# Kernel tuning notes

Hardware: AMD Instinct MI355X
Metric: run time of the kernel (lower is better)

## Reference

```python
import jax, jax.numpy as jnp
import numpy as np
from jax import lax

H = 1024       # hidden_size
I = 1024       # intermediate_size (per expert)
E = 16         # num_experts
TOP_K = 4      # num_active_experts


def setup_inputs() -> dict:
    key = jax.random.key(0)
    ks = jax.random.split(key, 9)
    std_gate = 0.02 / (E ** 0.5)
    return {
        "hidden_states": jax.random.normal(ks[0], (1, 2048, H), jnp.float32),
        "gate_w": jax.random.normal(ks[1], (E, H), jnp.float32) * std_gate,
        "expert_bias": jnp.zeros((E,), jnp.float32),
        "w1": jax.random.normal(ks[2], (E, I, H), jnp.float32) * 0.02,
        "w2": jax.random.normal(ks[3], (E, H, I), jnp.float32) * 0.02,
        "w3": jax.random.normal(ks[4], (E, I, H), jnp.float32) * 0.02,
        "sw1": jax.random.normal(ks[5], (I, H), jnp.float32) * 0.02,
        "sw2": jax.random.normal(ks[6], (H, I), jnp.float32) * 0.02,
        "sw3": jax.random.normal(ks[7], (I, H), jnp.float32) * 0.02,
    }


def _swiglu(x, wg, wd, wu):
    # Swish(x W1^T) * (x W3^T) then W2^T
    return (jax.nn.silu(x @ wg.T) * (x @ wu.T)) @ wd.T


def reference(hidden_states, gate_w, expert_bias, w1, w2, w3, sw1, sw2, sw3):
    B, S, Hd = hidden_states.shape
    x = hidden_states.reshape(-1, Hd)              # [T, H]
    T = x.shape[0]

    # ---- Router ----
    router_logits = x @ gate_w.T                   # [T, E]
    biased = router_logits + expert_bias           # loss-free balancing bias
    _, sel = lax.top_k(biased, TOP_K)              # [T, K] indices from biased logits
    raw = jnp.take_along_axis(router_logits, sel, axis=-1)  # weights from UNbiased logits
    rw = jax.nn.softmax(raw.astype(jnp.float32), axis=-1).astype(x.dtype)  # [T, K]

    # Dense combine weights g[t, e] = routing weight if e selected else 0
    g = jnp.zeros((T, E), x.dtype).at[jnp.arange(T)[:, None], sel].add(rw)

    # ---- Routed experts (mathematically equal to grouped dispatch) ----
    routed = jnp.zeros_like(x)
    for e in range(E):  # fixed small expert loop
        routed = routed + g[:, e:e + 1] * _swiglu(x, w1[e], w2[e], w3[e])

    # ---- Shared expert ----
    shared = _swiglu(x, sw1, sw2, sw3)

    out = (shared + routed).reshape(B, S, Hd)      # dropout p=0 -> identity
    return out
```

## Files before the change

### kernel.cpp

```cpp
#include <hip/hip_runtime.h>
#include <cstddef>
#include <cstdint>

#define T_TOK 2048
#define HD 1024
#define ID 1024
#define NE 16
#define TOPK 4
#define BM 128
#define BN 128
#define BK 32
#define MT_MAX 96
#define SLOT_CAP (MT_MAX * BM)

typedef float f32x4 __attribute__((ext_vector_type(4)));
typedef __bf16 bf16x8 __attribute__((ext_vector_type(8)));
typedef __bf16 bf16x4 __attribute__((ext_vector_type(4)));

#define WS_TILE_E 256
#define WS_LOGITS 4096
#define WS_SLOT_TOK (WS_LOGITS + T_TOK * NE * 4)
#define WS_SLOT_W (WS_SLOT_TOK + SLOT_CAP * 4)
#define WS_H1 (WS_SLOT_W + SLOT_CAP * 4)
#define WS_XB (WS_H1 + (size_t)SLOT_CAP * ID * 2)
#define WS_W1B (WS_XB + (size_t)T_TOK * HD * 2)
#define EXSZ ((size_t)ID * HD)

__device__ __forceinline__ f32x4 mfma16(bf16x8 a, bf16x8 b, f32x4 c) {
  return __builtin_amdgcn_mfma_f32_16x16x32_bf16(a, b, c, 0, 0, 0);
}

__device__ __forceinline__ bf16x4 pack4(f32x4 a) {
  bf16x4 o;
  o[0] = (__bf16)a[0]; o[1] = (__bf16)a[1]; o[2] = (__bf16)a[2]; o[3] = (__bf16)a[3];
  return o;
}

__device__ __forceinline__ void gload16(const __bf16* g, __bf16* l) {
  __builtin_amdgcn_global_load_lds(
      (const __attribute__((address_space(1))) uint32_t*)g,
      (__attribute__((address_space(3))) uint32_t*)l, 16, 0, 0);
}

__device__ __forceinline__ void cvt_chunk(const float* __restrict__ src,
                                          __bf16* __restrict__ dst, size_t off,
                                          int tid) {
  const f32x4* p = (const f32x4*)src + off + tid;
  __bf16* q = dst + 4 * (off + tid);
  f32x4 v0 = __builtin_nontemporal_load(p);
  f32x4 v1 = __builtin_nontemporal_load(p + 256);
  f32x4 v2 = __builtin_nontemporal_load(p + 512);
  f32x4 v3 = __builtin_nontemporal_load(p + 768);
  f32x4 v4 = __builtin_nontemporal_load(p + 1024);
  f32x4 v5 = __builtin_nontemporal_load(p + 1280);
  f32x4 v6 = __builtin_nontemporal_load(p + 1536);
  f32x4 v7 = __builtin_nontemporal_load(p + 1792);
  *(bf16x4*)(q + 0 * 1024) = pack4(v0);
  *(bf16x4*)(q + 1 * 1024) = pack4(v1);
  *(bf16x4*)(q + 2 * 1024) = pack4(v2);
  *(bf16x4*)(q + 3 * 1024) = pack4(v3);
  *(bf16x4*)(q + 4 * 1024) = pack4(v4);
  *(bf16x4*)(q + 5 * 1024) = pack4(v5);
  *(bf16x4*)(q + 6 * 1024) = pack4(v6);
  *(bf16x4*)(q + 7 * 1024) = pack4(v7);
}

#define W4 ((size_t)1 << 22)
#define S4 ((size_t)1 << 18)
#define X4 ((size_t)1 << 19)
#define CVT4_TOTAL (2 * W4 + 2 * S4 + X4)
#define NCHUNK (CVT4_TOTAL / 2048)
#define CVT_GRID 2048
#define LOGITS_BLOCKS (T_TOK / 4)

__global__ __launch_bounds__(256) void fused_pre(
    const float* __restrict__ w1, const float* __restrict__ w3,
    const float* __restrict__ sw1, const float* __restrict__ sw3,
    const float* __restrict__ x, __bf16* __restrict__ w1b,
    __bf16* __restrict__ w3b, __bf16* __restrict__ xb,
    const float* __restrict__ gw, float* __restrict__ logits) {
  int tid = threadIdx.x;
  if ((int)blockIdx.x < LOGITS_BLOCKS) {
    int wv = tid >> 6;
    int lane = tid & 63;
    int tok = blockIdx.x * 4 + wv;
    int e = lane >> 2;
    int q = lane & 3;
    const float4* xr = (const float4*)(x + (size_t)tok * HD) + q * 64;
    const float4* wr = (const float4*)(gw + (size_t)e * HD) + q * 64;
    float s0 = 0.f, s1 = 0.f;
#pragma unroll 8
    for (int i = 0; i < 64; i += 2) {
      float4 a0 = xr[i], w0 = wr[i];
      float4 a1 = xr[i + 1], w1v = wr[i + 1];
      s0 += a0.x * w0.x + a0.y * w0.y + a0.z * w0.z + a0.w * w0.w;
      s1 += a1.x * w1v.x + a1.y * w1v.y + a1.z * w1v.z + a1.w * w1v.w;
    }
    float s = s0 + s1;
    s += __shfl_xor(s, 1);
    s += __shfl_xor(s, 2);
    if (q == 0) logits[(size_t)tok * NE + e] = s;
    return;
  }
  size_t b = blockIdx.x - LOGITS_BLOCKS;
  for (size_t c = b; c < NCHUNK; c += CVT_GRID) {
    size_t f = c * 2048;
    const float* src;
    __bf16* dst;
    size_t off;
    if (f < W4) { src = w1; dst = w1b; off = f; }
    else if (f < 2 * W4) { src = w3; dst = w3b; off = f - W4; }
    else if (f < 2 * W4 + S4) { src = sw1; dst = w1b + 16 * EXSZ; off = f - 2 * W4; }
    else if (f < 2 * W4 + 2 * S4) { src = sw3; dst = w3b + 16 * EXSZ; off = f - 2 * W4 - S4; }
    else { src = x; dst = xb; off = f - 2 * W4 - 2 * S4; }
    cvt_chunk(src, dst, off, tid);
  }
}

__global__ __launch_bounds__(256) void router_finish(
    const float* __restrict__ logits, const float* __restrict__ bias,
    int* __restrict__ tile_e, int* __restrict__ slot_tok,
    float* __restrict__ slot_w) {
  __shared__ int hist[NE];
  __shared__ int soff[NE + 1];
  __shared__ int fillp[NE];
  __shared__ unsigned lsel[T_TOK];
  __shared__ float4 lw4[T_TOK];

  int tid = threadIdx.x;
  if (tid < NE) { hist[tid] = 0; fillp[tid] = 0; }
  __syncthreads();

  float bb[NE];
#pragma unroll
  for (int e = 0; e < NE; ++e) bb[e] = bias[e];

  for (int j = 0; j < T_TOK / 256; ++j) {
    int t = tid + 256 * j;
    float lg[NE];
    const float4* lp = (const float4*)(logits + (size_t)t * NE);
#pragma unroll
    for (int q = 0; q < 4; ++q) {
      float4 v = lp[q];
      lg[4 * q] = v.x; lg[4 * q + 1] = v.y; lg[4 * q + 2] = v.z; lg[4 * q + 3] = v.w;
    }
    float b[NE];
#pragma unroll
    for (int e = 0; e < NE; ++e) b[e] = lg[e] + bb[e];

    int selk[TOPK];
    float raw[TOPK];
    unsigned used = 0;
#pragma unroll
    for (int k = 0; k < TOPK; ++k) {
      float best = -3.4e38f;
      int bi = 0;
#pragma unroll
      for (int e = 0; e < NE; ++e) {
        if (!((used >> e) & 1) && b[e] > best) { best = b[e]; bi = e; }
      }
      used |= (1u << bi);
      selk[k] = bi;
      raw[k] = lg[bi];
    }
    float m = raw[0];
#pragma unroll
    for (int k = 1; k < TOPK; ++k) m = fmaxf(m, raw[k]);
    float s = 0.f;
    float w[TOPK];
#pragma unroll
    for (int k = 0; k < TOPK; ++k) { w[k] = __expf(raw[k] - m); s += w[k]; }
    float inv = 1.f / s;
    lsel[t] = (unsigned)selk[0] | ((unsigned)selk[1] << 8) |
              ((unsigned)selk[2] << 16) | ((unsigned)selk[3] << 24);
    lw4[t] = make_float4(w[0] * inv, w[1] * inv, w[2] * inv, w[3] * inv);
#pragma unroll
    for (int k = 0; k < TOPK; ++k) atomicAdd(&hist[selk[k]], 1);
  }
  __syncthreads();

  if (tid == 0) {
    int o = 0;
    for (int e = 0; e < NE; ++e) { soff[e] = o; o += (hist[e] + BM - 1) & ~(BM - 1); }
    soff[NE] = o;
  }
  __syncthreads();
  int shared_base = soff[NE];
  int total = shared_base + T_TOK;
  for (int tt = tid; tt < MT_MAX; tt += 256) {
    int base = tt * BM;
    int ee = -1;
    if (base < shared_base) {
      ee = 0;
#pragma unroll
      for (int q = 1; q < NE; ++q) if (base >= soff[q]) ee = q;
    } else if (base < total) {
      ee = NE;
    }
    tile_e[tt] = ee;
  }

  for (int j = 0; j < T_TOK / 256; ++j) {
    int t = tid + 256 * j;
    unsigned ps = lsel[t];
    float4 wv = lw4[t];
    int e0 = ps & 255, e1 = (ps >> 8) & 255, e2 = (ps >> 16) & 255, e3 = ps >> 24;
    int p0 = atomicAdd(&fillp[e0], 1);
    slot_tok[soff[e0] + p0] = t; slot_w[soff[e0] + p0] = wv.x;
    int p1 = atomicAdd(&fillp[e1], 1);
    slot_tok[soff[e1] + p1] = t; slot_w[soff[e1] + p1] = wv.y;
    int p2 = atomicAdd(&fillp[e2], 1);
    slot_tok[soff[e2] + p2] = t; slot_w[soff[e2] + p2] = wv.z;
    int p3 = atomicAdd(&fillp[e3], 1);
    slot_tok[soff[e3] + p3] = t; slot_w[soff[e3] + p3] = wv.w;
  }

  for (int s = tid; s < shared_base; s += 256) {
    int e = 0;
#pragma unroll
    for (int q = 1; q < NE; ++q) if (s >= soff[q]) e = q;
    if (s >= soff[e] + hist[e]) { slot_tok[s] = -1; slot_w[s] = 0.f; }
  }
  for (int s = shared_base + tid; s < total; s += 256) {
    slot_tok[s] = s - shared_base;
    slot_w[s] = 1.0f;
  }
}

#define P1_BLOCKS (8 * MT_MAX)
#define W2CHUNKS ((int)((W4 + S4) / 2048))

__global__ __launch_bounds__(256, 2) void pass1_bf16(
    const __bf16* __restrict__ xb, const int* __restrict__ slot_tok,
    const int* __restrict__ tile_e, const __bf16* __restrict__ w1b,
    const __bf16* __restrict__ w3b, __bf16* __restrict__ h1,
    const float* __restrict__ w2, const float* __restrict__ sw2,
    __bf16* __restrict__ w2b) {
  int tid = threadIdx.x;
  int bid = blockIdx.x;
  if (bid >= P1_BLOCKS) {
    size_t f = (size_t)(bid - P1_BLOCKS) * 2048;
    if (f < W4) cvt_chunk(w2, w2b, f, tid);
    else cvt_chunk(sw2, w2b + 16 * EXSZ, f - W4, tid);
    return;
  }
  int nt = bid & 7;
  int mt = bid >> 3;
  int e = tile_e[mt];
  if (e < 0) return;
  int n0 = nt * BN;
  int m0 = mt * BM;

  const __bf16* wg = w1b + (size_t)e * EXSZ;
  const __bf16* wu = w3b + (size_t)e * EXSZ;

  __shared__ __align__(16) __bf16 As[2][BM * BK];
  __shared__ __align__(16) __bf16 Bg[2][BN * BK];
  __shared__ __align__(16) __bf16 Bu[2][BN * BK];

  int r0 = tid >> 2, r1 = r0 + 64;
  int c8 = ((tid & 3) ^ ((r0 >> 1) & 3)) * 8;
  int tok0 = slot_tok[m0 + r0]; if (tok0 < 0) tok0 = 0;
  int tok1 = slot_tok[m0 + r1]; if (tok1 < 0) tok1 = 0;
  const __bf16* gA0 = xb + (size_t)tok0 * HD + c8;
  const __bf16* gA1 = xb + (size_t)tok1 * HD + c8;
  const __bf16* gG0 = wg + (size_t)(n0 + r0) * HD + c8;
  const __bf16* gG1 = wg + (size_t)(n0 + r1) * HD + c8;
  const __bf16* gU0 = wu + (size_t)(n0 + r0) * HD + c8;
  const __bf16* gU1 = wu + (size_t)(n0 + r1) * HD + c8;

  int wave = tid >> 6, lane = tid & 63;
  int wm = (wave >> 1) * 64, wn = (wave & 1) * 64;
  int l16 = lane & 15, kch = lane >> 4;
  int kk8 = (kch ^ ((l16 >> 1) & 3)) * 8;

  f32x4 accg[4][4] = {};
  f32x4 accu[4][4] = {};

  auto stage = [&](int B, int k0) {
    gload16(gA0 + k0, &As[B][(size_t)tid * 8]);
    gload16(gA1 + k0, &As[B][(size_t)(tid + 256) * 8]);
    gload16(gG0 + k0, &Bg[B][(size_t)tid * 8]);
    gload16(gG1 + k0, &Bg[B][(size_t)(tid + 256) * 8]);
    gload16(gU0 + k0, &Bu[B][(size_t)tid * 8]);
    gload16(gU1 + k0, &Bu[B][(size_t)(tid + 256) * 8]);
  };
  auto body = [&](int B) {
    bf16x8 af[4], gf[4], uf[4];
#pragma unroll
    for (int i = 0; i < 4; ++i) {
      af[i] = *(const bf16x8*)(&As[B][(wm + i * 16 + l16) * BK + kk8]);
      gf[i] = *(const bf16x8*)(&Bg[B][(wn + i * 16 + l16) * BK + kk8]);
      uf[i] = *(const bf16x8*)(&Bu[B][(wn + i * 16 + l16) * BK + kk8]);
    }
    asm volatile("s_waitcnt lgkmcnt(0)" ::: "memory");
    __builtin_amdgcn_s_barrier();
    __builtin_amdgcn_sched_barrier(0);
#pragma unroll
    for (int mi = 0; mi < 4; ++mi)
#pragma unroll
      for (int ni = 0; ni < 4; ++ni) {
        accg[mi][ni] = mfma16(af[mi], gf[ni], accg[mi][ni]);
        accu[mi][ni] = mfma16(af[mi], uf[ni], accu[mi][ni]);
      }
  };

  stage(0, 0);
#pragma unroll 1
  for (int k = 0; k < HD / BK - 1; ++k) {
    int cur = k & 1;
    stage(cur ^ 1, (k + 1) * BK);
    asm volatile("s_waitcnt vmcnt(6)" ::: "memory");
    __builtin_amdgcn_s_barrier();
    __builtin_amdgcn_sched_barrier(0);
    body(cur);
  }
  asm volatile("s_waitcnt vmcnt(0)" ::: "memory");
  __builtin_amdgcn_s_barrier();
  __builtin_amdgcn_sched_barrier(0);
  body((HD / BK - 1) & 1);

#pragma unroll
  for (int mi = 0; mi < 4; ++mi) {
#pragma unroll
    for (int ni = 0; ni < 4; ++ni) {
#pragma unroll
      for (int j = 0; j < 4; ++j) {
        int row = m0 + wm + mi * 16 + kch * 4 + j;
        int col = n0 + wn + ni * 16 + l16;
        float g = accg[mi][ni][j];
        float u = accu[mi][ni][j];
        float hv = (g / (1.f + __expf(-g))) * u;
        h1[(size_t)row * ID + col] = (__bf16)hv;
      }
    }
  }
}

__global__ __launch_bounds__(256, 3) void pass2_bf16(
    const __bf16* __restrict__ h1, const int* __restrict__ slot_tok,
    const float* __restrict__ slot_w, const int* __restrict__ tile_e,
    const __bf16* __restrict__ w2b, float* __restrict__ out) {
  int mt = blockIdx.y;
  int e = tile_e[mt];
  if (e < 0) return;
  int n0 = blockIdx.x * BN;
  int m0 = mt * BM;

  const __bf16* wd = w2b + (size_t)e * EXSZ;

  __shared__ __align__(16) __bf16 As[2][BM * BK];
  __shared__ __align__(16) __bf16 Bs[2][BN * BK];

  int tid = threadIdx.x;
  int r0 = tid >> 2, r1 = r0 + 64;
  int c8 = ((tid & 3) ^ ((r0 >> 1) & 3)) * 8;
  const __bf16* gA0 = h1 + (size_t)(m0 + r0) * ID + c8;
  const __bf16* gA1 = h1 + (size_t)(m0 + r1) * ID + c8;
  const __bf16* gB0 = wd + (size_t)(n0 + r0) * ID + c8;
  const __bf16* gB1 = wd + (size_t)(n0 + r1) * ID + c8;

  int wave = tid >> 6, lane = tid & 63;
  int wm = (wave >> 1) * 64, wn = (wave & 1) * 64;
  int l16 = lane & 15, kch = lane >> 4;
  int kk8 = (kch ^ ((l16 >> 1) & 3)) * 8;

  f32x4 acc[4][4] = {};

  auto stage = [&](int B, int k0) {
    gload16(gA0 + k0, &As[B][(size_t)tid * 8]);
    gload16(gA1 + k0, &As[B][(size_t)(tid + 256) * 8]);
    gload16(gB0 + k0, &Bs[B][(size_t)tid * 8]);
    gload16(gB1 + k0, &Bs[B][(size_t)(tid + 256) * 8]);
  };
  auto body = [&](int B) {
    bf16x8 af[4], bf[4];
#pragma unroll
    for (int i = 0; i < 4; ++i) {
      af[i] = *(const bf16x8*)(&As[B][(wm + i * 16 + l16) * BK + kk8]);
      bf[i] = *(const bf16x8*)(&Bs[B][(wn + i * 16 + l16) * BK + kk8]);
    }
    asm volatile("s_waitcnt lgkmcnt(0)" ::: "memory");
    __builtin_amdgcn_s_barrier();
    __builtin_amdgcn_sched_barrier(0);
#pragma unroll
    for (int mi = 0; mi < 4; ++mi)
#pragma unroll
      for (int ni = 0; ni < 4; ++ni)
        acc[mi][ni] = mfma16(af[mi], bf[ni], acc[mi][ni]);
  };

  stage(0, 0);
#pragma unroll 1
  for (int k = 0; k < ID / BK - 1; ++k) {
    int cur = k & 1;
    stage(cur ^ 1, (k + 1) * BK);
    asm volatile("s_waitcnt vmcnt(4)" ::: "memory");
    __builtin_amdgcn_s_barrier();
    __builtin_amdgcn_sched_barrier(0);
    body(cur);
  }
  asm volatile("s_waitcnt vmcnt(0)" ::: "memory");
  __builtin_amdgcn_s_barrier();
  __builtin_amdgcn_sched_barrier(0);
  body((ID / BK - 1) & 1);

#pragma unroll
  for (int mi = 0; mi < 4; ++mi) {
#pragma unroll
    for (int j = 0; j < 4; ++j) {
      int row = m0 + wm + mi * 16 + kch * 4 + j;
      int token = slot_tok[row];
      if (token < 0) continue;
      float wgt = slot_w[row];
#pragma unroll
      for (int ni = 0; ni < 4; ++ni) {
        int col = n0 + wn + ni * 16 + l16;
        atomicAdd(out + (size_t)token * HD + col, wgt * acc[mi][ni][j]);
      }
    }
  }
}

extern "C" void kernel_launch(void* const* d_in, const int* in_sizes, int n_in,
                              void* d_out, int out_size, void* d_ws, size_t ws_size,
                              hipStream_t stream) {
  const float* x = (const float*)d_in[0];
  const float* gate_w = (const float*)d_in[1];
  const float* ebias = (const float*)d_in[2];
  const float* w1 = (const float*)d_in[3];
  const float* w2 = (const float*)d_in[4];
  const float* w3 = (const float*)d_in[5];
  const float* sw1 = (const float*)d_in[6];
  const float* sw2 = (const float*)d_in[7];
  const float* sw3 = (const float*)d_in[8];
  float* out = (float*)d_out;

  char* ws = (char*)d_ws;
  int* tile_e = (int*)(ws + WS_TILE_E);
  float* logits = (float*)(ws + WS_LOGITS);
  int* slot_tok = (int*)(ws + WS_SLOT_TOK);
  float* slot_w = (float*)(ws + WS_SLOT_W);
  __bf16* h1 = (__bf16*)(ws + WS_H1);
  __bf16* xb = (__bf16*)(ws + WS_XB);
  __bf16* w1b = (__bf16*)(ws + WS_W1B);
  __bf16* w3b = w1b + 17 * EXSZ;
  __bf16* w2b = w3b + 17 * EXSZ;

  hipMemsetAsync(d_out, 0, (size_t)T_TOK * HD * sizeof(float), stream);

  fused_pre<<<LOGITS_BLOCKS + CVT_GRID, 256, 0, stream>>>(
      w1, w3, sw1, sw3, x, w1b, w3b, xb, gate_w, logits);
  router_finish<<<1, 256, 0, stream>>>(logits, ebias, tile_e, slot_tok, slot_w);

  pass1_bf16<<<P1_BLOCKS + W2CHUNKS, 256, 0, stream>>>(
      xb, slot_tok, tile_e, w1b, w3b, h1, w2, sw2, w2b);
  pass2_bf16<<<dim3(HD / BN, MT_MAX), 256, 0, stream>>>(
      h1, slot_tok, slot_w, tile_e, w2b, out);
}
```

Measured before the change: 234.1 us.

## Enlarge pass1 tiles to 256x128x64 with 512-thread blocks and per-expert 256-row padding

Pass1 (gate/up GEMM with SwiGLU) now uses 256-row M tiles, a K depth of 64 and 512 threads with 8 waves. Each wave computes 128x32 with an XOR-swizzled shared layout. Expert slot segments are padded to 256 rows, so router_finish emits a second tile map for pass1 while pass2 keeps 128-row tiles, with MT_MAX raised to 112. The piggybacked w2 conversion now handles 4096-float4 chunks per block using nontemporal loads. The aim is more weight reuse per loaded tile and fewer barriers, at the cost of extra padded rows per expert and lower occupancy from the larger LDS footprint.

```diff
diff --git a/kernel.cpp b/kernel.cpp
--- a/kernel.cpp
+++ b/kernel.cpp
@@ -10,14 +10,20 @@
 #define BM 128
 #define BN 128
 #define BK 32
-#define MT_MAX 96
-#define SLOT_CAP (MT_MAX * BM)
+#define BM1 256
+#define BN1 128
+#define BK1 64
+#define NK1 (HD / BK1)
+#define MT_MAX 112
+#define MT2_MAX 64
+#define SLOT_CAP 16384
 
 typedef float f32x4 __attribute__((ext_vector_type(4)));
 typedef __bf16 bf16x8 __attribute__((ext_vector_type(8)));
 typedef __bf16 bf16x4 __attribute__((ext_vector_type(4)));
 
 #define WS_TILE_E 256
+#define WS_TILE_E2 2048
 #define WS_LOGITS 4096
 #define WS_SLOT_TOK (WS_LOGITS + T_TOK * NE * 4)
 #define WS_SLOT_W (WS_SLOT_TOK + SLOT_CAP * 4)
@@ -119,8 +125,8 @@
 
 __global__ __launch_bounds__(256) void router_finish(
     const float* __restrict__ logits, const float* __restrict__ bias,
-    int* __restrict__ tile_e, int* __restrict__ slot_tok,
-    float* __restrict__ slot_w) {
+    int* __restrict__ tile_e, int* __restrict__ tile_e2,
+    int* __restrict__ slot_tok, float* __restrict__ slot_w) {
   __shared__ int hist[NE];
   __shared__ int soff[NE + 1];
   __shared__ int fillp[NE];
@@ -181,7 +187,7 @@
 
   if (tid == 0) {
     int o = 0;
-    for (int e = 0; e < NE; ++e) { soff[e] = o; o += (hist[e] + BM - 1) & ~(BM - 1); }
+    for (int e = 0; e < NE; ++e) { soff[e] = o; o += (hist[e] + BM1 - 1) & ~(BM1 - 1); }
     soff[NE] = o;
   }
   __syncthreads();
@@ -198,6 +204,18 @@
       ee = NE;
     }
     tile_e[tt] = ee;
+  }
+  for (int tt = tid; tt < MT2_MAX; tt += 256) {
+    int base = tt * BM1;
+    int ee = -1;
+    if (base < shared_base) {
+      ee = 0;
+#pragma unroll
+      for (int q = 1; q < NE; ++q) if (base >= soff[q]) ee = q;
+    } else if (base < total) {
+      ee = NE;
+    }
+    tile_e2[tt] = ee;
   }
 
   for (int j = 0; j < T_TOK / 256; ++j) {
@@ -227,103 +245,144 @@
   }
 }
 
-#define P1_BLOCKS (8 * MT_MAX)
-#define W2CHUNKS ((int)((W4 + S4) / 2048))
-
-__global__ __launch_bounds__(256, 2) void pass1_bf16(
+#define P1_BLOCKS (8 * MT2_MAX)
+#define W2CHUNKS ((int)((W4 + S4) / 4096))
+
+__global__ __launch_bounds__(512, 2) void pass1_bf16(
     const __bf16* __restrict__ xb, const int* __restrict__ slot_tok,
-    const int* __restrict__ tile_e, const __bf16* __restrict__ w1b,
+    const int* __restrict__ tile_e2, const __bf16* __restrict__ w1b,
     const __bf16* __restrict__ w3b, __bf16* __restrict__ h1,
     const float* __restrict__ w2, const float* __restrict__ sw2,
     __bf16* __restrict__ w2b) {
   int tid = threadIdx.x;
   int bid = blockIdx.x;
   if (bid >= P1_BLOCKS) {
-    size_t f = (size_t)(bid - P1_BLOCKS) * 2048;
-    if (f < W4) cvt_chunk(w2, w2b, f, tid);
-    else cvt_chunk(sw2, w2b + 16 * EXSZ, f - W4, tid);
+    size_t f = (size_t)(bid - P1_BLOCKS) * 4096;
+    const float* src;
+    __bf16* dst;
+    size_t off;
+    if (f < W4) { src = w2; dst = w2b; off = f; }
+    else { src = sw2; dst = w2b + 16 * EXSZ; off = f - W4; }
+    const f32x4* p = (const f32x4*)src + off + tid;
+    __bf16* q = dst + 4 * (off + tid);
+    f32x4 v0 = __builtin_nontemporal_load(p);
+    f32x4 v1 = __builtin_nontemporal_load(p + 512);
+    f32x4 v2 = __builtin_nontemporal_load(p + 1024);
+    f32x4 v3 = __builtin_nontemporal_load(p + 1536);
+    f32x4 v4 = __builtin_nontemporal_load(p + 2048);
+    f32x4 v5 = __builtin_nontemporal_load(p + 2560);
+    f32x4 v6 = __builtin_nontemporal_load(p + 3072);
+    f32x4 v7 = __builtin_nontemporal_load(p + 3584);
+    *(bf16x4*)(q + 0 * 2048) = pack4(v0);
+    *(bf16x4*)(q + 1 * 2048) = pack4(v1);
+    *(bf16x4*)(q + 2 * 2048) = pack4(v2);
+    *(bf16x4*)(q + 3 * 2048) = pack4(v3);
+    *(bf16x4*)(q + 4 * 2048) = pack4(v4);
+    *(bf16x4*)(q + 5 * 2048) = pack4(v5);
+    *(bf16x4*)(q + 6 * 2048) = pack4(v6);
+    *(bf16x4*)(q + 7 * 2048) = pack4(v7);
     return;
   }
   int nt = bid & 7;
   int mt = bid >> 3;
-  int e = tile_e[mt];
+  int e = tile_e2[mt];
   if (e < 0) return;
-  int n0 = nt * BN;
-  int m0 = mt * BM;
+  int n0 = nt * BN1;
+  int m0 = mt * BM1;
 
   const __bf16* wg = w1b + (size_t)e * EXSZ;
   const __bf16* wu = w3b + (size_t)e * EXSZ;
 
-  __shared__ __align__(16) __bf16 As[2][BM * BK];
-  __shared__ __align__(16) __bf16 Bg[2][BN * BK];
-  __shared__ __align__(16) __bf16 Bu[2][BN * BK];
-
-  int r0 = tid >> 2, r1 = r0 + 64;
-  int c8 = ((tid & 3) ^ ((r0 >> 1) & 3)) * 8;
-  int tok0 = slot_tok[m0 + r0]; if (tok0 < 0) tok0 = 0;
-  int tok1 = slot_tok[m0 + r1]; if (tok1 < 0) tok1 = 0;
-  const __bf16* gA0 = xb + (size_t)tok0 * HD + c8;
-  const __bf16* gA1 = xb + (size_t)tok1 * HD + c8;
-  const __bf16* gG0 = wg + (size_t)(n0 + r0) * HD + c8;
-  const __bf16* gG1 = wg + (size_t)(n0 + r1) * HD + c8;
-  const __bf16* gU0 = wu + (size_t)(n0 + r0) * HD + c8;
-  const __bf16* gU1 = wu + (size_t)(n0 + r1) * HD + c8;
+  __shared__ __align__(16) __bf16 As[2][BM1 * BK1];
+  __shared__ __align__(16) __bf16 Bg[2][BN1 * BK1];
+  __shared__ __align__(16) __bf16 Bu[2][BN1 * BK1];
+
+  const __bf16* gA[4];
+#pragma unroll
+  for (int j = 0; j < 4; ++j) {
+    int id = tid + j * 512;
+    int r = id >> 3;
+    int c = (id & 7) ^ (r & 7);
+    int tok = slot_tok[m0 + r];
+    if (tok < 0) tok = 0;
+    gA[j] = xb + (size_t)tok * HD + c * 8;
+  }
+  const __bf16* gG[2];
+  const __bf16* gU[2];
+#pragma unroll
+  for (int j = 0; j < 2; ++j) {
+    int id = tid + j * 512;
+    int r = id >> 3;
+    int c = (id & 7) ^ (r & 7);
+    gG[j] = wg + (size_t)(n0 + r) * HD + c * 8;
+    gU[j] = wu + (size_t)(n0 + r) * HD + c * 8;
+  }
 
   int wave = tid >> 6, lane = tid & 63;
-  int wm = (wave >> 1) * 64, wn = (wave & 1) * 64;
+  int wm = (wave >> 2) * 128;
+  int wn = (wave & 3) * 32;
   int l16 = lane & 15, kch = lane >> 4;
-  int kk8 = (kch ^ ((l16 >> 1) & 3)) * 8;
-
-  f32x4 accg[4][4] = {};
-  f32x4 accu[4][4] = {};
+
+  f32x4 accg[8][2] = {};
+  f32x4 accu[8][2] = {};
 
   auto stage = [&](int B, int k0) {
-    gload16(gA0 + k0, &As[B][(size_t)tid * 8]);
-    gload16(gA1 + k0, &As[B][(size_t)(tid + 256) * 8]);
-    gload16(gG0 + k0, &Bg[B][(size_t)tid * 8]);
-    gload16(gG1 + k0, &Bg[B][(size_t)(tid + 256) * 8]);
-    gload16(gU0 + k0, &Bu[B][(size_t)tid * 8]);
-    gload16(gU1 + k0, &Bu[B][(size_t)(tid + 256) * 8]);
+#pragma unroll
+    for (int j = 0; j < 4; ++j)
+      gload16(gA[j] + k0, &As[B][(size_t)(tid + j * 512) * 8]);
+#pragma unroll
+    for (int j = 0; j < 2; ++j) {
+      gload16(gG[j] + k0, &Bg[B][(size_t)(tid + j * 512) * 8]);
+      gload16(gU[j] + k0, &Bu[B][(size_t)(tid + j * 512) * 8]);
+    }
   };
-  auto body = [&](int B) {
-    bf16x8 af[4], gf[4], uf[4];
-#pragma unroll
-    for (int i = 0; i < 4; ++i) {
-      af[i] = *(const bf16x8*)(&As[B][(wm + i * 16 + l16) * BK + kk8]);
-      gf[i] = *(const bf16x8*)(&Bg[B][(wn + i * 16 + l16) * BK + kk8]);
-      uf[i] = *(const bf16x8*)(&Bu[B][(wn + i * 16 + l16) * BK + kk8]);
-    }
-    asm volatile("s_waitcnt lgkmcnt(0)" ::: "memory");
+
+#pragma unroll 1
+  for (int k = 0; k < NK1; ++k) {
+    int buf = k & 1;
+    if (k == 0) stage(0, 0);
+    if (k + 1 < NK1) {
+      stage(buf ^ 1, (k + 1) * BK1);
+      asm volatile("s_waitcnt vmcnt(8)" ::: "memory");
+    } else {
+      asm volatile("s_waitcnt vmcnt(0)" ::: "memory");
+    }
     __builtin_amdgcn_s_barrier();
     __builtin_amdgcn_sched_barrier(0);
-#pragma unroll
-    for (int mi = 0; mi < 4; ++mi)
-#pragma unroll
-      for (int ni = 0; ni < 4; ++ni) {
-        accg[mi][ni] = mfma16(af[mi], gf[ni], accg[mi][ni]);
-        accu[mi][ni] = mfma16(af[mi], uf[ni], accu[mi][ni]);
+
+#pragma unroll
+    for (int s = 0; s < 2; ++s) {
+      bf16x8 af[8], gf[2], uf[2];
+#pragma unroll
+      for (int i = 0; i < 8; ++i) {
+        int R = wm + i * 16 + l16;
+        int c = s * 4 + kch;
+        af[i] = *(const bf16x8*)(&As[buf][R * BK1 + ((c ^ (R & 7)) * 8)]);
       }
-  };
-
-  stage(0, 0);
-#pragma unroll 1
-  for (int k = 0; k < HD / BK - 1; ++k) {
-    int cur = k & 1;
-    stage(cur ^ 1, (k + 1) * BK);
-    asm volatile("s_waitcnt vmcnt(6)" ::: "memory");
-    __builtin_amdgcn_s_barrier();
-    __builtin_amdgcn_sched_barrier(0);
-    body(cur);
-  }
-  asm volatile("s_waitcnt vmcnt(0)" ::: "memory");
-  __builtin_amdgcn_s_barrier();
-  __builtin_amdgcn_sched_barrier(0);
-  body((HD / BK - 1) & 1);
-
-#pragma unroll
-  for (int mi = 0; mi < 4; ++mi) {
-#pragma unroll
-    for (int ni = 0; ni < 4; ++ni) {
+#pragma unroll
+      for (int i = 0; i < 2; ++i) {
+        int R = wn + i * 16 + l16;
+        int c = s * 4 + kch;
+        gf[i] = *(const bf16x8*)(&Bg[buf][R * BK1 + ((c ^ (R & 7)) * 8)]);
+        uf[i] = *(const bf16x8*)(&Bu[buf][R * BK1 + ((c ^ (R & 7)) * 8)]);
+      }
+      asm volatile("s_waitcnt lgkmcnt(0)" ::: "memory");
+      if (s == 1) __builtin_amdgcn_s_barrier();
+      __builtin_amdgcn_sched_barrier(0);
+#pragma unroll
+      for (int mi = 0; mi < 8; ++mi)
+#pragma unroll
+        for (int ni = 0; ni < 2; ++ni) {
+          accg[mi][ni] = mfma16(af[mi], gf[ni], accg[mi][ni]);
+          accu[mi][ni] = mfma16(af[mi], uf[ni], accu[mi][ni]);
+        }
+    }
+  }
+
+#pragma unroll
+  for (int mi = 0; mi < 8; ++mi) {
+#pragma unroll
+    for (int ni = 0; ni < 2; ++ni) {
 #pragma unroll
       for (int j = 0; j < 4; ++j) {
         int row = m0 + wm + mi * 16 + kch * 4 + j;
@@ -438,6 +497,7 @@
 
   char* ws = (char*)d_ws;
   int* tile_e = (int*)(ws + WS_TILE_E);
+  int* tile_e2 = (int*)(ws + WS_TILE_E2);
   float* logits = (float*)(ws + WS_LOGITS);
   int* slot_tok = (int*)(ws + WS_SLOT_TOK);
   float* slot_w = (float*)(ws + WS_SLOT_W);
@@ -451,10 +511,11 @@
 
   fused_pre<<<LOGITS_BLOCKS + CVT_GRID, 256, 0, stream>>>(
       w1, w3, sw1, sw3, x, w1b, w3b, xb, gate_w, logits);
-  router_finish<<<1, 256, 0, stream>>>(logits, ebias, tile_e, slot_tok, slot_w);
-
-  pass1_bf16<<<P1_BLOCKS + W2CHUNKS, 256, 0, stream>>>(
-      xb, slot_tok, tile_e, w1b, w3b, h1, w2, sw2, w2b);
+  router_finish<<<1, 256, 0, stream>>>(logits, ebias, tile_e, tile_e2, slot_tok,
+                                       slot_w);
+
+  pass1_bf16<<<P1_BLOCKS + W2CHUNKS, 512, 0, stream>>>(
+      xb, slot_tok, tile_e2, w1b, w3b, h1, w2, sw2, w2b);
   pass2_bf16<<<dim3(HD / BN, MT_MAX), 256, 0, stream>>>(
       h1, slot_tok, slot_w, tile_e, w2b, out);
 }
```

New measurement: 228.8 us. 1.02x faster.
